# Optimization experiments

Hardware: AMD Instinct MI355X
Metric: run time of the kernel (lower is better)

Reference implementation:

```python
import jax, jax.numpy as jnp
import numpy as np

B, S, D = 16, 2048, 128  # batch*heads, seq_len, head_dim


def setup_inputs() -> dict:
    key = jax.random.key(0)
    kq, kk, kv, ks = jax.random.split(key, 4)
    q = jax.random.normal(kq, (B, S, D), dtype=jnp.float32)
    k = jax.random.normal(kk, (B, S, D), dtype=jnp.float32)
    v = jax.random.normal(kv, (B, S, D), dtype=jnp.float32)
    # full-shape scale tensor; keep values away from zero (~sqrt(D))
    inv_scale_factor = jax.random.uniform(ks, (B, S, S), dtype=jnp.float32,
                                          minval=8.0, maxval=16.0)
    return {"q": q, "k": k, "v": v,
            "inv_scale_factor": inv_scale_factor,
            "dropout_p": 0}


def reference(q, k, v, inv_scale_factor, dropout_p):
    # qk = q @ k^T  -> [B, Sq, Skv]
    qk = jnp.einsum('bqd,bkd->bqk', q, k)
    # elementwise divide by full-shape tensor (blocks fused SDPA dispatch)
    scaled_qk = qk / inv_scale_factor
    attn = jax.nn.softmax(scaled_qk, axis=-1)
    # dropout with p=0 is the identity (F.dropout scales by 1/(1-p) == 1)
    y = jnp.einsum('bqk,bkd->bqd', attn, v)
    return y
```

## Files before the change

kernel.cpp:

```cpp
#include <hip/hip_runtime.h>
#include <hip/hip_bf16.h>

#define BATCH 16
#define SEQ   2048
#define HD    128
#define QBLK  64
#define KVBLK 32
#define NT    (SEQ / KVBLK)
#define NW    4

typedef __attribute__((ext_vector_type(8))) short bf16x8;
typedef __attribute__((ext_vector_type(4))) float f32x4;
typedef __attribute__((ext_vector_type(4))) short s16x4;

__device__ __forceinline__ short f2bf(float x) {
    __hip_bfloat16 h = __float2bfloat16(x);
    return *reinterpret_cast<short*>(&h);
}

__global__ __launch_bounds__(256, 2)
void attn_fused(const float* __restrict__ Q, const float* __restrict__ K,
                const float* __restrict__ V, const float* __restrict__ ISF,
                float* __restrict__ O)
{
    const int tid  = threadIdx.x;
    const int lane = tid & 63;
    const int wv   = tid >> 6;
    const int lg   = lane >> 4;
    const int lc   = lane & 15;

    const int bidx = blockIdx.x;
    const int b    = bidx >> 5;
    const int q0   = (bidx & 31) * QBLK;

    __shared__ short Klds[2][32 * 128];
    __shared__ short Vtlds[2][128 * 40];
    __shared__ short Plds[NW * 16 * 40];

    bf16x8 qf[4];
    {
        const float* qrow = Q + ((size_t)b * SEQ + q0 + wv * 16 + lc) * HD;
        #pragma unroll
        for (int ks = 0; ks < 4; ++ks) {
            const float* p = qrow + ks * 32 + lg * 8;
            float4 x0 = *reinterpret_cast<const float4*>(p);
            float4 x1 = *reinterpret_cast<const float4*>(p + 4);
            bf16x8 f;
            f[0]=f2bf(x0.x); f[1]=f2bf(x0.y); f[2]=f2bf(x0.z); f[3]=f2bf(x0.w);
            f[4]=f2bf(x1.x); f[5]=f2bf(x1.y); f[6]=f2bf(x1.z); f[7]=f2bf(x1.w);
            qf[ks] = f;
        }
    }

    f32x4 oacc[8];
    #pragma unroll
    for (int i = 0; i < 8; ++i) oacc[i] = (f32x4){0.f, 0.f, 0.f, 0.f};
    float l_part[4] = {0.f, 0.f, 0.f, 0.f};

    const float* kbase = K + (size_t)b * SEQ * HD;
    const float* vbase = V + (size_t)b * SEQ * HD;
    const float* ibase = ISF + ((size_t)b * SEQ + q0 + wv * 16) * SEQ;

    float4 kreg[4];
    float  vreg[4][4];
    float  isf_cur[8], isf_nxt[8];

    auto LOAD = [&](int kv0) {
        const float* kb = kbase + (size_t)kv0 * HD;
        const float* vb = vbase + (size_t)kv0 * HD;
        #pragma unroll
        for (int r = 0; r < 4; ++r) {
            int idx = r * 256 + tid;
            kreg[r] = *reinterpret_cast<const float4*>(kb + (size_t)(idx >> 5) * HD + (idx & 31) * 4);
        }
        #pragma unroll
        for (int r = 0; r < 4; ++r) {
            int idx = r * 256 + tid;
            int d = idx & 127, kq = idx >> 7;
            #pragma unroll
            for (int j = 0; j < 4; ++j)
                vreg[r][j] = vb[(size_t)(kq * 4 + j) * HD + d];
        }
    };
    auto LOAD_ISF = [&](int kv0, float* dst) {
        #pragma unroll
        for (int nt = 0; nt < 2; ++nt)
            #pragma unroll
            for (int r = 0; r < 4; ++r)
                dst[nt * 4 + r] = ibase[(size_t)(lg * 4 + r) * SEQ + kv0 + nt * 16 + lc];
    };
    auto STORE = [&](int buf) {
        #pragma unroll
        for (int r = 0; r < 4; ++r) {
            int idx = r * 256 + tid;
            int kvr = idx >> 5, d4 = idx & 31;
            s16x4 s;
            s[0]=f2bf(kreg[r].x); s[1]=f2bf(kreg[r].y); s[2]=f2bf(kreg[r].z); s[3]=f2bf(kreg[r].w);
            int chunk = (d4 >> 1) ^ (kvr & 7);
            *reinterpret_cast<s16x4*>(&Klds[buf][kvr * 128 + chunk * 8 + (d4 & 1) * 4]) = s;
        }
        #pragma unroll
        for (int r = 0; r < 4; ++r) {
            int idx = r * 256 + tid;
            int d = idx & 127, kq = idx >> 7;
            s16x4 s;
            #pragma unroll
            for (int j = 0; j < 4; ++j) s[j] = f2bf(vreg[r][j]);
            *reinterpret_cast<s16x4*>(&Vtlds[buf][d * 40 + kq * 4]) = s;
        }
    };

    LOAD(0);
    LOAD_ISF(0, isf_nxt);
    STORE(0);
    __syncthreads();
    #pragma unroll
    for (int i = 0; i < 8; ++i)
        isf_cur[i] = __builtin_amdgcn_rcpf(isf_nxt[i]) * 1.44269504f;

    int cur = 0;
    for (int t = 0; t < NT; ++t) {
        const int kv0n = (t + 1) * KVBLK;
        const bool more = (t + 1 < NT);
        if (more) { LOAD(kv0n); LOAD_ISF(kv0n, isf_nxt); }

        f32x4 sacc[2];
        sacc[0] = (f32x4){0.f,0.f,0.f,0.f};
        sacc[1] = (f32x4){0.f,0.f,0.f,0.f};
        __builtin_amdgcn_s_setprio(1);
        #pragma unroll
        for (int nt = 0; nt < 2; ++nt) {
            int n = lc + nt * 16;
            #pragma unroll
            for (int ks = 0; ks < 4; ++ks) {
                int chunk = (ks * 4 + lg) ^ (n & 7);
                bf16x8 bf = *reinterpret_cast<const bf16x8*>(&Klds[cur][n * 128 + chunk * 8]);
                sacc[nt] = __builtin_amdgcn_mfma_f32_16x16x32_bf16(qf[ks], bf, sacc[nt], 0, 0, 0);
            }
        }
        __builtin_amdgcn_s_setprio(0);

        short pb[2][4];
        #pragma unroll
        for (int nt = 0; nt < 2; ++nt)
            #pragma unroll
            for (int r = 0; r < 4; ++r) {
                float p = __builtin_amdgcn_exp2f(sacc[nt][r] * isf_cur[nt * 4 + r]);
                l_part[r] += p;
                pb[nt][r] = f2bf(p);
            }

        short* pw = &Plds[wv * 16 * 40];
        #pragma unroll
        for (int nt = 0; nt < 2; ++nt)
            #pragma unroll
            for (int r = 0; r < 4; ++r)
                pw[(lg * 4 + r) * 40 + nt * 16 + lc] = pb[nt][r];
        bf16x8 pa = *reinterpret_cast<const bf16x8*>(&pw[lc * 40 + lg * 8]);

        __builtin_amdgcn_s_setprio(1);
        #pragma unroll
        for (int dt = 0; dt < 8; ++dt) {
            bf16x8 vf = *reinterpret_cast<const bf16x8*>(&Vtlds[cur][(lc + dt * 16) * 40 + lg * 8]);
            oacc[dt] = __builtin_amdgcn_mfma_f32_16x16x32_bf16(pa, vf, oacc[dt], 0, 0, 0);
        }
        __builtin_amdgcn_s_setprio(0);

        if (more) STORE(cur ^ 1);
        __syncthreads();
        cur ^= 1;
        #pragma unroll
        for (int i = 0; i < 8; ++i)
            isf_cur[i] = __builtin_amdgcn_rcpf(isf_nxt[i]) * 1.44269504f;
    }

    #pragma unroll
    for (int msk = 1; msk < 16; msk <<= 1)
        #pragma unroll
        for (int r = 0; r < 4; ++r)
            l_part[r] += __shfl_xor(l_part[r], msk, 64);

    float* ob = O + ((size_t)b * SEQ + q0 + wv * 16) * HD;
    #pragma unroll
    for (int r = 0; r < 4; ++r) {
        float inv_l = 1.0f / l_part[r];
        float* orow = ob + (size_t)(lg * 4 + r) * HD;
        #pragma unroll
        for (int dt = 0; dt < 8; ++dt)
            orow[lc + dt * 16] = oacc[dt][r] * inv_l;
    }
}

extern "C" void kernel_launch(void* const* d_in, const int* in_sizes, int n_in,
                              void* d_out, int out_size, void* d_ws, size_t ws_size,
                              hipStream_t stream) {
    const float* q   = (const float*)d_in[0];
    const float* k   = (const float*)d_in[1];
    const float* v   = (const float*)d_in[2];
    const float* isf = (const float*)d_in[3];
    float* out = (float*)d_out;
    dim3 grid(BATCH * (SEQ / QBLK));
    attn_fused<<<grid, 256, 0, stream>>>(q, k, v, isf, out);
}
```

Measured before the change: 111.3 us.

## Pre-convert K to bf16 and V to transposed bf16 in workspace before attention

Two small pre-pass kernels convert K to bf16 and V to a transposed bf16 layout in the workspace buffer, once per call. The attention kernel then loads 16-byte bf16 vectors straight into LDS instead of each of 32 query blocks per batch re-reading and re-converting fp32 K/V with strided scalar V loads. This halves K/V global traffic in the main loop and removes conversion ALU work, at the cost of two extra launches and a workspace round trip. The ISF stream (the dominant traffic) is unchanged.

Result: slower. 116.8 us (+4.9%).

```diff
diff --git a/kernel.cpp b/kernel.cpp
--- a/kernel.cpp
+++ b/kernel.cpp
@@ -18,9 +18,37 @@
     return *reinterpret_cast<short*>(&h);
 }
 
+__global__ __launch_bounds__(256)
+void cvt_k(const float* __restrict__ K, short* __restrict__ Kb)
+{
+    int c = blockIdx.x * 256 + threadIdx.x;
+    float4 x = reinterpret_cast<const float4*>(K)[c];
+    s16x4 s;
+    s[0] = f2bf(x.x); s[1] = f2bf(x.y); s[2] = f2bf(x.z); s[3] = f2bf(x.w);
+    reinterpret_cast<s16x4*>(Kb)[c] = s;
+}
+
+__global__ __launch_bounds__(256)
+void cvt_vt(const float* __restrict__ V, short* __restrict__ Vt)
+{
+    int c  = blockIdx.x * 256 + threadIdx.x;
+    int d  = c & 127;
+    int st = (c >> 7) & 127;
+    int b  = c >> 14;
+    const float* vb = V + ((size_t)b * SEQ + st * 16) * HD + d;
+    bf16x8 o0, o1;
+    #pragma unroll
+    for (int i = 0; i < 8; ++i) o0[i] = f2bf(vb[(size_t)i * HD]);
+    #pragma unroll
+    for (int i = 0; i < 8; ++i) o1[i] = f2bf(vb[(size_t)(i + 8) * HD]);
+    short* ob = Vt + ((size_t)b * HD + d) * SEQ + st * 16;
+    *reinterpret_cast<bf16x8*>(ob)     = o0;
+    *reinterpret_cast<bf16x8*>(ob + 8) = o1;
+}
+
 __global__ __launch_bounds__(256, 2)
-void attn_fused(const float* __restrict__ Q, const float* __restrict__ K,
-                const float* __restrict__ V, const float* __restrict__ ISF,
+void attn_fused(const float* __restrict__ Q, const short* __restrict__ Kb,
+                const short* __restrict__ Vt, const float* __restrict__ ISF,
                 float* __restrict__ O)
 {
     const int tid  = threadIdx.x;
@@ -57,29 +85,25 @@
     for (int i = 0; i < 8; ++i) oacc[i] = (f32x4){0.f, 0.f, 0.f, 0.f};
     float l_part[4] = {0.f, 0.f, 0.f, 0.f};
 
-    const float* kbase = K + (size_t)b * SEQ * HD;
-    const float* vbase = V + (size_t)b * SEQ * HD;
+    const short* kbase = Kb + (size_t)b * SEQ * HD;
+    const short* vbase = Vt + (size_t)b * HD * SEQ;
     const float* ibase = ISF + ((size_t)b * SEQ + q0 + wv * 16) * SEQ;
 
-    float4 kreg[4];
-    float  vreg[4][4];
+    bf16x8 kreg[2], vreg[2];
     float  isf_cur[8], isf_nxt[8];
 
     auto LOAD = [&](int kv0) {
-        const float* kb = kbase + (size_t)kv0 * HD;
-        const float* vb = vbase + (size_t)kv0 * HD;
-        #pragma unroll
-        for (int r = 0; r < 4; ++r) {
-            int idx = r * 256 + tid;
-            kreg[r] = *reinterpret_cast<const float4*>(kb + (size_t)(idx >> 5) * HD + (idx & 31) * 4);
-        }
-        #pragma unroll
-        for (int r = 0; r < 4; ++r) {
-            int idx = r * 256 + tid;
-            int d = idx & 127, kq = idx >> 7;
-            #pragma unroll
-            for (int j = 0; j < 4; ++j)
-                vreg[r][j] = vb[(size_t)(kq * 4 + j) * HD + d];
+        const short* kb = kbase + (size_t)kv0 * HD;
+        #pragma unroll
+        for (int r = 0; r < 2; ++r) {
+            int idx = r * 256 + tid;
+            kreg[r] = *reinterpret_cast<const bf16x8*>(kb + (idx >> 4) * HD + (idx & 15) * 8);
+        }
+        const short* vb = vbase + kv0;
+        #pragma unroll
+        for (int r = 0; r < 2; ++r) {
+            int idx = r * 256 + tid;
+            vreg[r] = *reinterpret_cast<const bf16x8*>(vb + (size_t)(idx >> 2) * SEQ + (idx & 3) * 8);
         }
     };
     auto LOAD_ISF = [&](int kv0, float* dst) {
@@ -91,22 +115,16 @@
     };
     auto STORE = [&](int buf) {
         #pragma unroll
-        for (int r = 0; r < 4; ++r) {
-            int idx = r * 256 + tid;
-            int kvr = idx >> 5, d4 = idx & 31;
-            s16x4 s;
-            s[0]=f2bf(kreg[r].x); s[1]=f2bf(kreg[r].y); s[2]=f2bf(kreg[r].z); s[3]=f2bf(kreg[r].w);
-            int chunk = (d4 >> 1) ^ (kvr & 7);
-            *reinterpret_cast<s16x4*>(&Klds[buf][kvr * 128 + chunk * 8 + (d4 & 1) * 4]) = s;
-        }
-        #pragma unroll
-        for (int r = 0; r < 4; ++r) {
-            int idx = r * 256 + tid;
-            int d = idx & 127, kq = idx >> 7;
-            s16x4 s;
-            #pragma unroll
-            for (int j = 0; j < 4; ++j) s[j] = f2bf(vreg[r][j]);
-            *reinterpret_cast<s16x4*>(&Vtlds[buf][d * 40 + kq * 4]) = s;
+        for (int r = 0; r < 2; ++r) {
+            int idx = r * 256 + tid;
+            int kvr = idx >> 4, dc = idx & 15;
+            *reinterpret_cast<bf16x8*>(&Klds[buf][kvr * 128 + (dc ^ (kvr & 7)) * 8]) = kreg[r];
+        }
+        #pragma unroll
+        for (int r = 0; r < 2; ++r) {
+            int idx = r * 256 + tid;
+            int d = idx >> 2, c = idx & 3;
+            *reinterpret_cast<bf16x8*>(&Vtlds[buf][d * 40 + c * 8]) = vreg[r];
         }
     };
 
@@ -199,6 +217,11 @@
     const float* v   = (const float*)d_in[2];
     const float* isf = (const float*)d_in[3];
     float* out = (float*)d_out;
-    dim3 grid(BATCH * (SEQ / QBLK));
-    attn_fused<<<grid, 256, 0, stream>>>(q, k, v, isf, out);
-}
+
+    const size_t kv_elems = (size_t)BATCH * SEQ * HD;
+    short* kb = (short*)d_ws;
+    short* vt = kb + kv_elems;
+    cvt_k <<<dim3(kv_elems / 4 / 256), 256, 0, stream>>>(k, kb);
+    cvt_vt<<<dim3(kv_elems / 16 / 256), 256, 0, stream>>>(v, vt);
+    attn_fused<<<dim3(BATCH * (SEQ / QBLK)), 256, 0, stream>>>(q, kb, vt, isf, out);
+}
```

## Split KV range across two blocks per query tile and merge partials

Applied to the files above, without the earlier changes.

Templates the fused attention kernel so each 64-row query tile is processed by two blocks, each covering half of the KV sequence. The blocks write unnormalized output partials and row sums to workspace, and a separate merge kernel adds them and normalizes. The aim is to double the number of blocks for more parallelism and latency hiding. In exchange it adds extra workspace traffic for the partials, a second kernel launch, and depends on the workspace being large enough, falling back to the single-pass kernel otherwise.

Result: slower. 123.4 us (+10.8%).

```diff
diff --git a/kernel.cpp b/kernel.cpp
--- a/kernel.cpp
+++ b/kernel.cpp
@@ -6,7 +6,6 @@
 #define HD    128
 #define QBLK  64
 #define KVBLK 32
-#define NT    (SEQ / KVBLK)
 #define NW    4
 
 typedef __attribute__((ext_vector_type(8))) short bf16x8;
@@ -18,10 +17,12 @@
     return *reinterpret_cast<short*>(&h);
 }
 
+template<int NTILES, bool PARTIAL>
 __global__ __launch_bounds__(256, 2)
 void attn_fused(const float* __restrict__ Q, const float* __restrict__ K,
                 const float* __restrict__ V, const float* __restrict__ ISF,
-                float* __restrict__ O)
+                float* __restrict__ O, float* __restrict__ opart,
+                float* __restrict__ lsum)
 {
     const int tid  = threadIdx.x;
     const int lane = tid & 63;
@@ -30,8 +31,10 @@
     const int lc   = lane & 15;
 
     const int bidx = blockIdx.x;
-    const int b    = bidx >> 5;
-    const int q0   = (bidx & 31) * QBLK;
+    const int qt   = PARTIAL ? (bidx >> 1) : bidx;
+    const int kvb  = PARTIAL ? ((bidx & 1) * (NTILES * KVBLK)) : 0;
+    const int b    = qt >> 5;
+    const int q0   = (qt & 31) * QBLK;
 
     __shared__ short Klds[2][32 * 128];
     __shared__ short Vtlds[2][128 * 40];
@@ -110,8 +113,8 @@
         }
     };
 
-    LOAD(0);
-    LOAD_ISF(0, isf_nxt);
+    LOAD(kvb);
+    LOAD_ISF(kvb, isf_nxt);
     STORE(0);
     __syncthreads();
     #pragma unroll
@@ -119,9 +122,9 @@
         isf_cur[i] = __builtin_amdgcn_rcpf(isf_nxt[i]) * 1.44269504f;
 
     int cur = 0;
-    for (int t = 0; t < NT; ++t) {
-        const int kv0n = (t + 1) * KVBLK;
-        const bool more = (t + 1 < NT);
+    for (int t = 0; t < NTILES; ++t) {
+        const bool more = (t + 1 < NTILES);
+        const int kv0n = kvb + (t + 1) * KVBLK;
         if (more) { LOAD(kv0n); LOAD_ISF(kv0n, isf_nxt); }
 
         f32x4 sacc[2];
@@ -180,15 +183,49 @@
         for (int r = 0; r < 4; ++r)
             l_part[r] += __shfl_xor(l_part[r], msk, 64);
 
-    float* ob = O + ((size_t)b * SEQ + q0 + wv * 16) * HD;
-    #pragma unroll
-    for (int r = 0; r < 4; ++r) {
-        float inv_l = 1.0f / l_part[r];
-        float* orow = ob + (size_t)(lg * 4 + r) * HD;
-        #pragma unroll
-        for (int dt = 0; dt < 8; ++dt)
-            orow[lc + dt * 16] = oacc[dt][r] * inv_l;
-    }
+    if (PARTIAL) {
+        const size_t rowbase = (size_t)bidx * 64 + wv * 16;
+        #pragma unroll
+        for (int r = 0; r < 4; ++r) {
+            float* orow = opart + (rowbase + lg * 4 + r) * HD;
+            #pragma unroll
+            for (int dt = 0; dt < 8; ++dt)
+                orow[lc + dt * 16] = oacc[dt][r];
+            if (lc == 0) lsum[rowbase + lg * 4 + r] = l_part[r];
+        }
+    } else {
+        float* ob = O + ((size_t)b * SEQ + q0 + wv * 16) * HD;
+        #pragma unroll
+        for (int r = 0; r < 4; ++r) {
+            float inv_l = 1.0f / l_part[r];
+            float* orow = ob + (size_t)(lg * 4 + r) * HD;
+            #pragma unroll
+            for (int dt = 0; dt < 8; ++dt)
+                orow[lc + dt * 16] = oacc[dt][r] * inv_l;
+        }
+    }
+}
+
+__global__ __launch_bounds__(256)
+void merge_k(const float* __restrict__ opart, const float* __restrict__ lsum,
+             float* __restrict__ O)
+{
+    int gid = blockIdx.x * 256 + threadIdx.x;
+    int row = gid >> 5;
+    int c4  = gid & 31;
+    int qt  = row >> 6;
+    int rin = row & 63;
+    size_t i0 = (size_t)(2 * qt) * 64 + rin;
+    size_t i1 = i0 + 64;
+    float inv = 1.0f / (lsum[i0] + lsum[i1]);
+    float4 o0 = reinterpret_cast<const float4*>(opart)[i0 * 32 + c4];
+    float4 o1 = reinterpret_cast<const float4*>(opart)[i1 * 32 + c4];
+    float4 out;
+    out.x = (o0.x + o1.x) * inv;
+    out.y = (o0.y + o1.y) * inv;
+    out.z = (o0.z + o1.z) * inv;
+    out.w = (o0.w + o1.w) * inv;
+    reinterpret_cast<float4*>(O)[(size_t)row * 32 + c4] = out;
 }
 
 extern "C" void kernel_launch(void* const* d_in, const int* in_sizes, int n_in,
@@ -199,6 +236,16 @@
     const float* v   = (const float*)d_in[2];
     const float* isf = (const float*)d_in[3];
     float* out = (float*)d_out;
-    dim3 grid(BATCH * (SEQ / QBLK));
-    attn_fused<<<grid, 256, 0, stream>>>(q, k, v, isf, out);
-}
+
+    const size_t opart_elems = (size_t)1024 * 64 * HD;
+    const size_t lsum_elems  = (size_t)1024 * 64;
+    const size_t need = (opart_elems + lsum_elems) * sizeof(float);
+    if (ws_size >= need) {
+        float* opart = (float*)d_ws;
+        float* lsum  = opart + opart_elems;
+        attn_fused<32, true><<<dim3(1024), 256, 0, stream>>>(q, k, v, isf, out, opart, lsum);
+        merge_k<<<dim3(4096), 256, 0, stream>>>(opart, lsum, out);
+    } else {
+        attn_fused<64, false><<<dim3(512), 256, 0, stream>>>(q, k, v, isf, out, out, out);
+    }
+}
```

## Transpose QK^T MFMA and shuffle P in registers instead of LDS

Applied to the files above, without the earlier changes.

Swaps the MFMA operands so each lane holds scores for one query row across four consecutive key columns. This lets the scale tensor be read as float4 vectors instead of strided scalar loads, and the row-sum needs a single accumulator. The P tile is rearranged into the A-operand layout with cross-lane shuffles instead of a round-trip through shared memory. The QK accumulation is also split into two independent chains to shorten MFMA dependency latency. The shuffle and select logic adds VALU work, and its lane mapping must be exactly right for correctness.

Measured after the change: 118.3 us. 6.3% more time.

```diff
diff --git a/kernel.cpp b/kernel.cpp
--- a/kernel.cpp
+++ b/kernel.cpp
@@ -7,7 +7,6 @@
 #define QBLK  64
 #define KVBLK 32
 #define NT    (SEQ / KVBLK)
-#define NW    4
 
 typedef __attribute__((ext_vector_type(8))) short bf16x8;
 typedef __attribute__((ext_vector_type(4))) float f32x4;
@@ -35,7 +34,6 @@
 
     __shared__ short Klds[2][32 * 128];
     __shared__ short Vtlds[2][128 * 40];
-    __shared__ short Plds[NW * 16 * 40];
 
     bf16x8 qf[4];
     {
@@ -55,15 +53,16 @@
     f32x4 oacc[8];
     #pragma unroll
     for (int i = 0; i < 8; ++i) oacc[i] = (f32x4){0.f, 0.f, 0.f, 0.f};
-    float l_part[4] = {0.f, 0.f, 0.f, 0.f};
+    float l_part = 0.f;
 
     const float* kbase = K + (size_t)b * SEQ * HD;
     const float* vbase = V + (size_t)b * SEQ * HD;
-    const float* ibase = ISF + ((size_t)b * SEQ + q0 + wv * 16) * SEQ;
+    const float* ibase = ISF + ((size_t)b * SEQ + q0 + wv * 16 + lc) * SEQ;
 
     float4 kreg[4];
     float  vreg[4][4];
-    float  isf_cur[8], isf_nxt[8];
+    float4 isf_nxt[2];
+    float  isf_cur[8];
 
     auto LOAD = [&](int kv0) {
         const float* kb = kbase + (size_t)kv0 * HD;
@@ -82,12 +81,10 @@
                 vreg[r][j] = vb[(size_t)(kq * 4 + j) * HD + d];
         }
     };
-    auto LOAD_ISF = [&](int kv0, float* dst) {
+    auto LOAD_ISF = [&](int kv0) {
         #pragma unroll
         for (int nt = 0; nt < 2; ++nt)
-            #pragma unroll
-            for (int r = 0; r < 4; ++r)
-                dst[nt * 4 + r] = ibase[(size_t)(lg * 4 + r) * SEQ + kv0 + nt * 16 + lc];
+            isf_nxt[nt] = *reinterpret_cast<const float4*>(ibase + kv0 + nt * 16 + lg * 4);
     };
     auto STORE = [&](int buf) {
         #pragma unroll
@@ -111,22 +108,31 @@
     };
 
     LOAD(0);
-    LOAD_ISF(0, isf_nxt);
+    LOAD_ISF(0);
     STORE(0);
     __syncthreads();
     #pragma unroll
-    for (int i = 0; i < 8; ++i)
-        isf_cur[i] = __builtin_amdgcn_rcpf(isf_nxt[i]) * 1.44269504f;
+    for (int nt = 0; nt < 2; ++nt)
+        #pragma unroll
+        for (int r = 0; r < 4; ++r)
+            isf_cur[nt * 4 + r] = __builtin_amdgcn_rcpf(isf_nxt[nt][r]) * 1.44269504f;
+
+    const int srcA = lc + 16 * (2 * (lg & 1) + (lg >> 1));
+    const int srcB = lc + 16 * (2 * (lg & 1) + 1 - (lg >> 1));
+    const bool hi  = (lg >> 1) != 0;
 
     int cur = 0;
     for (int t = 0; t < NT; ++t) {
         const int kv0n = (t + 1) * KVBLK;
         const bool more = (t + 1 < NT);
-        if (more) { LOAD(kv0n); LOAD_ISF(kv0n, isf_nxt); }
-
-        f32x4 sacc[2];
-        sacc[0] = (f32x4){0.f,0.f,0.f,0.f};
-        sacc[1] = (f32x4){0.f,0.f,0.f,0.f};
+        if (more) { LOAD(kv0n); LOAD_ISF(kv0n); }
+
+        f32x4 sacc[2], sacc2[2];
+        #pragma unroll
+        for (int nt = 0; nt < 2; ++nt) {
+            sacc[nt]  = (f32x4){0.f,0.f,0.f,0.f};
+            sacc2[nt] = (f32x4){0.f,0.f,0.f,0.f};
+        }
         __builtin_amdgcn_s_setprio(1);
         #pragma unroll
         for (int nt = 0; nt < 2; ++nt) {
@@ -135,28 +141,45 @@
             for (int ks = 0; ks < 4; ++ks) {
                 int chunk = (ks * 4 + lg) ^ (n & 7);
                 bf16x8 bf = *reinterpret_cast<const bf16x8*>(&Klds[cur][n * 128 + chunk * 8]);
-                sacc[nt] = __builtin_amdgcn_mfma_f32_16x16x32_bf16(qf[ks], bf, sacc[nt], 0, 0, 0);
+                if (ks < 2) sacc[nt]  = __builtin_amdgcn_mfma_f32_16x16x32_bf16(bf, qf[ks], sacc[nt],  0, 0, 0);
+                else        sacc2[nt] = __builtin_amdgcn_mfma_f32_16x16x32_bf16(bf, qf[ks], sacc2[nt], 0, 0, 0);
             }
         }
         __builtin_amdgcn_s_setprio(0);
 
-        short pb[2][4];
+        float p[2][4];
+        #pragma unroll
+        for (int nt = 0; nt < 2; ++nt) {
+            f32x4 s4 = sacc[nt] + sacc2[nt];
+            #pragma unroll
+            for (int r = 0; r < 4; ++r)
+                p[nt][r] = __builtin_amdgcn_exp2f(s4[r] * isf_cur[nt * 4 + r]);
+        }
+        l_part += ((p[0][0] + p[0][1]) + (p[0][2] + p[0][3]))
+                + ((p[1][0] + p[1][1]) + (p[1][2] + p[1][3]));
+
+        unsigned pk[2][2];
         #pragma unroll
         for (int nt = 0; nt < 2; ++nt)
             #pragma unroll
-            for (int r = 0; r < 4; ++r) {
-                float p = __builtin_amdgcn_exp2f(sacc[nt][r] * isf_cur[nt * 4 + r]);
-                l_part[r] += p;
-                pb[nt][r] = f2bf(p);
-            }
-
-        short* pw = &Plds[wv * 16 * 40];
-        #pragma unroll
-        for (int nt = 0; nt < 2; ++nt)
-            #pragma unroll
-            for (int r = 0; r < 4; ++r)
-                pw[(lg * 4 + r) * 40 + nt * 16 + lc] = pb[nt][r];
-        bf16x8 pa = *reinterpret_cast<const bf16x8*>(&pw[lc * 40 + lg * 8]);
+            for (int s = 0; s < 2; ++s)
+                pk[nt][s] = (unsigned)(unsigned short)f2bf(p[nt][2 * s])
+                          | ((unsigned)(unsigned short)f2bf(p[nt][2 * s + 1]) << 16);
+
+        unsigned vA0 = (lg & 1) ? pk[1][0] : pk[0][0];
+        unsigned vA1 = (lg & 1) ? pk[1][1] : pk[0][1];
+        unsigned vB0 = (lg & 1) ? pk[0][0] : pk[1][0];
+        unsigned vB1 = (lg & 1) ? pk[0][1] : pk[1][1];
+        unsigned rA0 = (unsigned)__shfl((int)vA0, srcA);
+        unsigned rA1 = (unsigned)__shfl((int)vA1, srcA);
+        unsigned rB0 = (unsigned)__shfl((int)vB0, srcB);
+        unsigned rB1 = (unsigned)__shfl((int)vB1, srcB);
+        union { unsigned u[4]; bf16x8 v; } pau;
+        pau.u[0] = hi ? rB0 : rA0;
+        pau.u[1] = hi ? rB1 : rA1;
+        pau.u[2] = hi ? rA0 : rB0;
+        pau.u[3] = hi ? rA1 : rB1;
+        bf16x8 pa = pau.v;
 
         __builtin_amdgcn_s_setprio(1);
         #pragma unroll
@@ -170,20 +193,19 @@
         __syncthreads();
         cur ^= 1;
         #pragma unroll
-        for (int i = 0; i < 8; ++i)
-            isf_cur[i] = __builtin_amdgcn_rcpf(isf_nxt[i]) * 1.44269504f;
+        for (int nt = 0; nt < 2; ++nt)
+            #pragma unroll
+            for (int r = 0; r < 4; ++r)
+                isf_cur[nt * 4 + r] = __builtin_amdgcn_rcpf(isf_nxt[nt][r]) * 1.44269504f;
     }
 
-    #pragma unroll
-    for (int msk = 1; msk < 16; msk <<= 1)
-        #pragma unroll
-        for (int r = 0; r < 4; ++r)
-            l_part[r] += __shfl_xor(l_part[r], msk, 64);
+    l_part += __shfl_xor(l_part, 16, 64);
+    l_part += __shfl_xor(l_part, 32, 64);
 
     float* ob = O + ((size_t)b * SEQ + q0 + wv * 16) * HD;
     #pragma unroll
     for (int r = 0; r < 4; ++r) {
-        float inv_l = 1.0f / l_part[r];
+        float inv_l = 1.0f / __shfl(l_part, lg * 4 + r, 64);
         float* orow = ob + (size_t)(lg * 4 + r) * HD;
         #pragma unroll
         for (int dt = 0; dt < 8; ++dt)
```
